# Performance work log

Measured on AMD Instinct MI355X. Metric: run time of the kernel, lower is better.

The kernel has to match this reference:

```python
import jax, jax.numpy as jnp
import numpy as np

DIM = 1024
HEADS = 16
DIM_HEAD = 64
INNER = HEADS * DIM_HEAD
B, N = 2, 2048


def setup_inputs() -> dict:
    key = jax.random.key(0)
    ks = jax.random.split(key, 5)
    x = jax.random.normal(ks[0], (B, N, DIM), dtype=jnp.float32)
    ln_gamma = jnp.ones((DIM,), dtype=jnp.float32)
    ln_beta = jnp.zeros((DIM,), dtype=jnp.float32)
    # torch Linear: weight [out, in]; store as [in, out] for x @ W
    W_qkv = jax.random.normal(ks[1], (DIM, 3 * INNER), dtype=jnp.float32) * (DIM ** -0.5)
    W_out = jax.random.normal(ks[2], (INNER, DIM), dtype=jnp.float32) * (INNER ** -0.5)
    b_out = jax.random.normal(ks[3], (DIM,), dtype=jnp.float32) * 0.01
    return {"x": x, "ln_gamma": ln_gamma, "ln_beta": ln_beta,
            "W_qkv": W_qkv, "W_out": W_out, "b_out": b_out}


def reference(x, ln_gamma, ln_beta, W_qkv, W_out, b_out):
    eps = 1e-5
    scale = DIM_HEAD ** -0.5
    # LayerNorm over last dim
    mu = jnp.mean(x, axis=-1, keepdims=True)
    var = jnp.mean((x - mu) ** 2, axis=-1, keepdims=True)
    xn = (x - mu) * jax.lax.rsqrt(var + eps) * ln_gamma + ln_beta
    # QKV projection (no bias), split
    qkv = xn @ W_qkv                               # [B, N, 3*inner]
    q, k, v = jnp.split(qkv, 3, axis=-1)           # each [B, N, inner]
    def heads(t):
        return t.reshape(B, N, HEADS, DIM_HEAD).transpose(0, 2, 1, 3)  # [B, H, N, d]
    q, k, v = heads(q), heads(k), heads(v)
    dots = jnp.einsum("bhnd,bhmd->bhnm", q, k) * scale
    a = jax.nn.softmax(dots, axis=-1)
    out = jnp.einsum("bhnm,bhmd->bhnd", a, v)      # [B, H, N, d]
    out = out.transpose(0, 2, 1, 3).reshape(B, N, INNER)
    return out @ W_out + b_out                     # dropout p=0 -> identity
```

## Files before the change

kernel.cpp:

```cpp
#include <hip/hip_runtime.h>

typedef unsigned short U16;
typedef __bf16 bf16x8 __attribute__((ext_vector_type(8)));
typedef float f32x4 __attribute__((ext_vector_type(4)));
typedef float f32x16 __attribute__((ext_vector_type(16)));

__device__ inline float b2f(U16 u) {
    union { unsigned int i; float f; } v;
    v.i = ((unsigned int)u) << 16;
    return v.f;
}
__device__ inline U16 f2b(float f) {
    union { float f; unsigned int u; } v;
    v.f = f;
    unsigned int r = (v.u + 0x7fffu + ((v.u >> 16) & 1u)) >> 16;
    return (U16)r;
}

__device__ inline unsigned cvt_pk(float lo, float hi) {
    unsigned d;
    asm("v_cvt_pk_bf16_f32 %0, %1, %2" : "=v"(d) : "v"(lo), "v"(hi));
    return d;
}
__device__ inline void plswap(unsigned &a, unsigned &b) {
    asm("v_permlane32_swap_b32 %0, %1" : "+v"(a), "+v"(b));
}

__device__ inline void gld16(const void* g, void* l) {
    __builtin_amdgcn_global_load_lds(
        (const __attribute__((address_space(1))) void*)g,
        (__attribute__((address_space(3))) void*)l, 16, 0, 0);
}

__global__ void transpose2_f2b(const float* __restrict__ inA, U16* __restrict__ outA,
                               int RA, int CA,
                               const float* __restrict__ inB, U16* __restrict__ outB,
                               int RB, int CB) {
    const float* in; U16* out; int R, C;
    if (blockIdx.z == 0) { in = inA; out = outA; R = RA; C = CA; }
    else {
        if ((int)blockIdx.x * 32 >= CB) return;
        in = inB; out = outB; R = RB; C = CB;
    }
    __shared__ float tile[32][33];
    int c0 = blockIdx.x * 32, r0 = blockIdx.y * 32;
    int tx = threadIdx.x, ty = threadIdx.y;
#pragma unroll
    for (int i = 0; i < 32; i += 8)
        tile[ty + i][tx] = in[(size_t)(r0 + ty + i) * C + c0 + tx];
    __syncthreads();
#pragma unroll
    for (int i = 0; i < 32; i += 8)
        out[(size_t)(c0 + ty + i) * R + r0 + tx] = f2b(tile[tx][ty + i]);
}

__global__ __launch_bounds__(256) void ln_kernel(const float* __restrict__ x,
                                                 const float* __restrict__ gamma,
                                                 const float* __restrict__ beta,
                                                 U16* __restrict__ xn) {
    int row = blockIdx.x;
    int t = threadIdx.x;
    float4 raw = ((const float4*)(x + (size_t)row * 1024))[t];
    float v[4] = { raw.x, raw.y, raw.z, raw.w };
    float s = v[0] + v[1] + v[2] + v[3];
    float s2 = v[0] * v[0] + v[1] * v[1] + v[2] * v[2] + v[3] * v[3];
#pragma unroll
    for (int off = 32; off >= 1; off >>= 1) {
        s  += __shfl_xor(s,  off);
        s2 += __shfl_xor(s2, off);
    }
    __shared__ float red[8];
    if ((t & 63) == 0) { red[(t >> 6) * 2] = s; red[(t >> 6) * 2 + 1] = s2; }
    __syncthreads();
    float S  = red[0] + red[2] + red[4] + red[6];
    float S2 = red[1] + red[3] + red[5] + red[7];
    float mu = S * (1.0f / 1024.0f);
    float var = S2 * (1.0f / 1024.0f) - mu * mu;
    float rstd = rsqrtf(var + 1e-5f);
    float4 g4 = ((const float4*)gamma)[t];
    float4 b4 = ((const float4*)beta)[t];
    ushort4 o;
    o.x = f2b((v[0] - mu) * rstd * g4.x + b4.x);
    o.y = f2b((v[1] - mu) * rstd * g4.y + b4.y);
    o.z = f2b((v[2] - mu) * rstd * g4.z + b4.z);
    o.w = f2b((v[3] - mu) * rstd * g4.w + b4.w);
    ((ushort4*)(xn + (size_t)row * 1024))[t] = o;
}

template <typename OutT>
__global__ __launch_bounds__(256) void gemm_bt(const U16* __restrict__ A,
                                               const U16* __restrict__ Bt,
                                               const float* __restrict__ bias,
                                               OutT* __restrict__ C,
                                               U16* __restrict__ vT,
                                               int M, int N, int K) {
    __shared__ __align__(16) U16 As[128 * 32];
    __shared__ __align__(16) U16 Bs[128 * 32];
    const int m0 = blockIdx.y * 128, n0 = blockIdx.x * 128;
    const int t = threadIdx.x;
    const int wave = t >> 6, lane = t & 63, l15 = lane & 15, quad = lane >> 4;
    const int wm = (wave >> 1) * 64, wn = (wave & 1) * 64;

    f32x4 acc[4][4];
#pragma unroll
    for (int i = 0; i < 4; i++)
#pragma unroll
        for (int j = 0; j < 4; j++)
            acc[i][j] = (f32x4){0.f, 0.f, 0.f, 0.f};

    const int c0i = t, c1i = 256 + t;
    const int r0 = c0i >> 2, kq0 = c0i & 3;
    const int r1 = c1i >> 2, kq1 = c1i & 3;

    for (int k0 = 0; k0 < K; k0 += 32) {
        gld16(&A[(size_t)(m0 + r0) * K + k0 + kq0 * 8], &As[c0i * 8]);
        gld16(&Bt[(size_t)(n0 + r0) * K + k0 + kq0 * 8], &Bs[c0i * 8]);
        gld16(&A[(size_t)(m0 + r1) * K + k0 + kq1 * 8], &As[c1i * 8]);
        gld16(&Bt[(size_t)(n0 + r1) * K + k0 + kq1 * 8], &Bs[c1i * 8]);
        __syncthreads();
        bf16x8 af[4], bfr[4];
#pragma unroll
        for (int i = 0; i < 4; i++)
            af[i] = *(const bf16x8*)&As[(wm + i * 16 + l15) * 32 + quad * 8];
#pragma unroll
        for (int j = 0; j < 4; j++)
            bfr[j] = *(const bf16x8*)&Bs[(wn + j * 16 + l15) * 32 + quad * 8];
#pragma unroll
        for (int i = 0; i < 4; i++)
#pragma unroll
            for (int j = 0; j < 4; j++)
                acc[i][j] = __builtin_amdgcn_mfma_f32_16x16x32_bf16(
                    af[i], bfr[j], acc[i][j], 0, 0, 0);
        __syncthreads();
    }
    if (vT && n0 >= 2048) {
#pragma unroll
        for (int i = 0; i < 4; i++) {
#pragma unroll
            for (int j = 0; j < 4; j++) {
                int col = n0 + wn + j * 16 + l15 - 2048;
                int hh = col >> 6, dd = col & 63;
                int row0 = m0 + wm + i * 16 + quad * 4;
                int bb = row0 >> 11, nn = row0 & 2047;
                ushort4 st;
                st.x = f2b(acc[i][j][0]); st.y = f2b(acc[i][j][1]);
                st.z = f2b(acc[i][j][2]); st.w = f2b(acc[i][j][3]);
                *(ushort4*)&vT[((((size_t)bb * 16) + hh) * 64 + dd) * 2048 + nn] = st;
            }
        }
        return;
    }
#pragma unroll
    for (int i = 0; i < 4; i++) {
#pragma unroll
        for (int j = 0; j < 4; j++) {
            int col = n0 + wn + j * 16 + l15;
            float bv = bias ? bias[col] : 0.0f;
#pragma unroll
            for (int r = 0; r < 4; r++) {
                int row = m0 + wm + i * 16 + quad * 4 + r;
                float val = acc[i][j][r] + bv;
                if constexpr (sizeof(OutT) == 4)
                    C[(size_t)row * N + col] = val;
                else
                    C[(size_t)row * N + col] = f2b(val);
            }
        }
    }
}

__global__ __launch_bounds__(256) void gemm_bt2(const U16* __restrict__ A,
                                                const U16* __restrict__ Bt,
                                                const float* __restrict__ bias,
                                                float* __restrict__ C,
                                                int M, int N, int K) {
    __shared__ __align__(16) U16 As[64 * 32];
    __shared__ __align__(16) U16 Bs[128 * 32];
    const int m0 = blockIdx.y * 64, n0 = blockIdx.x * 128;
    const int t = threadIdx.x;
    const int wave = t >> 6, lane = t & 63, l15 = lane & 15, quad = lane >> 4;
    const int wm = (wave >> 1) * 32, wn = (wave & 1) * 64;

    f32x4 acc[2][4];
#pragma unroll
    for (int i = 0; i < 2; i++)
#pragma unroll
        for (int j = 0; j < 4; j++)
            acc[i][j] = (f32x4){0.f, 0.f, 0.f, 0.f};

    const int rA = t >> 2, kqA = t & 3;

    for (int k0 = 0; k0 < K; k0 += 32) {
        gld16(&A[(size_t)(m0 + rA) * K + k0 + kqA * 8], &As[t * 8]);
        gld16(&Bt[(size_t)(n0 + rA) * K + k0 + kqA * 8], &Bs[t * 8]);
        gld16(&Bt[(size_t)(n0 + 64 + rA) * K + k0 + kqA * 8], &Bs[(256 + t) * 8]);
        __syncthreads();
        bf16x8 af[2], bfr[4];
#pragma unroll
        for (int i = 0; i < 2; i++)
            af[i] = *(const bf16x8*)&As[(wm + i * 16 + l15) * 32 + quad * 8];
#pragma unroll
        for (int j = 0; j < 4; j++)
            bfr[j] = *(const bf16x8*)&Bs[(wn + j * 16 + l15) * 32 + quad * 8];
#pragma unroll
        for (int i = 0; i < 2; i++)
#pragma unroll
            for (int j = 0; j < 4; j++)
                acc[i][j] = __builtin_amdgcn_mfma_f32_16x16x32_bf16(
                    af[i], bfr[j], acc[i][j], 0, 0, 0);
        __syncthreads();
    }
#pragma unroll
    for (int i = 0; i < 2; i++) {
#pragma unroll
        for (int j = 0; j < 4; j++) {
            int col = n0 + wn + j * 16 + l15;
            float bv = bias[col];
#pragma unroll
            for (int r = 0; r < 4; r++) {
                int row = m0 + wm + i * 16 + quad * 4 + r;
                C[(size_t)row * N + col] = acc[i][j][r] + bv;
            }
        }
    }
}

__global__ __launch_bounds__(256) void attn_kernel(const U16* __restrict__ qkv,
                                                   const U16* __restrict__ vT,
                                                   U16* __restrict__ attn_out) {
    const int p = blockIdx.x;
    const int xcd = p & 7;
    const int slot = p >> 3;
    const int bh = ((slot & 3) << 3) | xcd;
    const int qt = slot >> 2;
    const int b = bh >> 4, h = bh & 15;
    const int t = threadIdx.x;
    const int wave = t >> 6, lane = t & 63;
    const int l31 = lane & 31, hi = lane >> 5;
    const float sc2 = 0.125f * 1.44269504089f;

    __shared__ __align__(16) U16 Kt[2][64 * 64];
    __shared__ __align__(16) U16 Vt[2][64 * 64];

    const size_t base = (size_t)(b * 2048) * 3072;
    const U16* vTbh = vT + ((size_t)(b * 16 + h) * 64) * 2048;

    bf16x8 qf[4];
    {
        int qrow = qt * 128 + wave * 32 + l31;
        const U16* qp = qkv + base + (size_t)qrow * 3072 + h * 64 + hi * 8;
#pragma unroll
        for (int s = 0; s < 4; s++) {
            union { bf16x8 v; U16 u[8]; } a;
            a.v = *(const bf16x8*)&qp[s * 16];
#pragma unroll
            for (int e = 0; e < 8; e++) a.u[e] = f2b(b2f(a.u[e]) * sc2);
            qf[s] = a.v;
        }
    }

    float l4[4] = { 0.f, 0.f, 0.f, 0.f };
    f32x16 oacc[2];
#pragma unroll
    for (int db = 0; db < 2; db++)
#pragma unroll
        for (int r = 0; r < 16; r++)
            oacc[db][r] = 0.0f;

    const int c0 = t, c1 = 256 + t;
    const int row0 = c0 >> 3, oct0 = (c0 & 7) ^ (row0 & 7);
    const int row1 = c1 >> 3, oct1 = (c1 & 7) ^ (row1 & 7);

    gld16(&qkv[base + (size_t)row0 * 3072 + 1024 + h * 64 + oct0 * 8], &Kt[0][c0 * 8]);
    gld16(&qkv[base + (size_t)row1 * 3072 + 1024 + h * 64 + oct1 * 8], &Kt[0][c1 * 8]);
    gld16(&vTbh[(size_t)row0 * 2048 + oct0 * 8], &Vt[0][c0 * 8]);
    gld16(&vTbh[(size_t)row1 * 2048 + oct1 * 8], &Vt[0][c1 * 8]);
    __syncthreads();

    auto step = [&](const U16* KtC, const U16* VtC, U16* KtN, U16* VtN, int nt) {
        gld16(&qkv[base + (size_t)(nt * 64 + row0) * 3072 + 1024 + h * 64 + oct0 * 8], &KtN[c0 * 8]);
        gld16(&qkv[base + (size_t)(nt * 64 + row1) * 3072 + 1024 + h * 64 + oct1 * 8], &KtN[c1 * 8]);
        gld16(&vTbh[(size_t)row0 * 2048 + nt * 64 + oct0 * 8], &VtN[c0 * 8]);
        gld16(&vTbh[(size_t)row1 * 2048 + nt * 64 + oct1 * 8], &VtN[c1 * 8]);
#pragma unroll
        for (int kb = 0; kb < 2; kb++) {
            bf16x8 kf[4];
#pragma unroll
            for (int s = 0; s < 4; s++)
                kf[s] = *(const bf16x8*)&KtC[(kb * 32 + l31) * 64 +
                                             (((s * 2 + hi) ^ (l31 & 7)) * 8)];
            bf16x8 vfr[2][2];
#pragma unroll
            for (int db = 0; db < 2; db++)
#pragma unroll
                for (int s = 0; s < 2; s++)
                    vfr[db][s] = *(const bf16x8*)&VtC[(db * 32 + l31) * 64 +
                                                      (((kb * 4 + s * 2 + hi) ^ (l31 & 7)) * 8)];

            f32x16 st = {0.f, 0.f, 0.f, 0.f, 0.f, 0.f, 0.f, 0.f,
                         0.f, 0.f, 0.f, 0.f, 0.f, 0.f, 0.f, 0.f};
            __builtin_amdgcn_s_setprio(1);
#pragma unroll
            for (int s = 0; s < 4; s++)
                st = __builtin_amdgcn_mfma_f32_32x32x16_bf16(kf[s], qf[s], st, 0, 0, 0);
            __builtin_amdgcn_s_setprio(0);

            float pe[16];
#pragma unroll
            for (int r = 0; r < 16; r++) {
                pe[r] = __builtin_amdgcn_exp2f(st[r]);
                l4[r & 3] += pe[r];
            }

#pragma unroll
            for (int s = 0; s < 2; s++) {
                unsigned p01 = cvt_pk(pe[s * 8 + 0], pe[s * 8 + 1]);
                unsigned p23 = cvt_pk(pe[s * 8 + 2], pe[s * 8 + 3]);
                unsigned p45 = cvt_pk(pe[s * 8 + 4], pe[s * 8 + 5]);
                unsigned p67 = cvt_pk(pe[s * 8 + 6], pe[s * 8 + 7]);
                plswap(p01, p45);
                plswap(p23, p67);
                union { unsigned u[4]; bf16x8 v; } pw;
                pw.u[0] = p01; pw.u[1] = p23; pw.u[2] = p45; pw.u[3] = p67;
                __builtin_amdgcn_s_setprio(1);
#pragma unroll
                for (int db = 0; db < 2; db++)
                    oacc[db] = __builtin_amdgcn_mfma_f32_32x32x16_bf16(
                        vfr[db][s], pw.v, oacc[db], 0, 0, 0);
                __builtin_amdgcn_s_setprio(0);
            }
        }
        __syncthreads();
    };

    for (int kt2 = 0; kt2 < 16; kt2++) {
        step(&Kt[0][0], &Vt[0][0], &Kt[1][0], &Vt[1][0], 2 * kt2 + 1);
        step(&Kt[1][0], &Vt[1][0], &Kt[0][0], &Vt[0][0], (2 * kt2 + 2) & 31);
    }

    float l_acc = (l4[0] + l4[1]) + (l4[2] + l4[3]);
    float lt = l_acc + __shfl_xor(l_acc, 32);
    float inv = 1.0f / lt;
    int qrow = b * 2048 + qt * 128 + wave * 32 + l31;
#pragma unroll
    for (int db = 0; db < 2; db++) {
#pragma unroll
        for (int g = 0; g < 4; g++) {
            ushort4 stv;
            stv.x = f2b(oacc[db][g * 4 + 0] * inv);
            stv.y = f2b(oacc[db][g * 4 + 1] * inv);
            stv.z = f2b(oacc[db][g * 4 + 2] * inv);
            stv.w = f2b(oacc[db][g * 4 + 3] * inv);
            int col = h * 64 + db * 32 + g * 8 + hi * 4;
            *(ushort4*)&attn_out[(size_t)qrow * 1024 + col] = stv;
        }
    }
}

extern "C" void kernel_launch(void* const* d_in, const int* in_sizes, int n_in,
                              void* d_out, int out_size, void* d_ws, size_t ws_size,
                              hipStream_t stream) {
    (void)in_sizes; (void)n_in; (void)out_size; (void)ws_size;
    const float* x    = (const float*)d_in[0];
    const float* g    = (const float*)d_in[1];
    const float* be   = (const float*)d_in[2];
    const float* Wqkv = (const float*)d_in[3];
    const float* Wout = (const float*)d_in[4];
    const float* bout = (const float*)d_in[5];
    float* out = (float*)d_out;
    char* ws = (char*)d_ws;

    U16* xn   = (U16*)(ws);
    U16* qkv  = (U16*)(ws + (size_t)(8u  << 20));
    U16* WqT  = (U16*)(ws + (size_t)(32u << 20));
    U16* WoT  = (U16*)(ws + (size_t)(38u << 20));
    U16* vT   = (U16*)(ws + (size_t)(40u << 20));
    U16* aout = xn;

    transpose2_f2b<<<dim3(3072 / 32, 1024 / 32, 2), dim3(32, 8), 0, stream>>>(
        Wqkv, WqT, 1024, 3072, Wout, WoT, 1024, 1024);
    ln_kernel<<<4096, 256, 0, stream>>>(x, g, be, xn);
    gemm_bt<U16><<<dim3(3072 / 128, 4096 / 128), 256, 0, stream>>>(xn, WqT, nullptr, qkv, vT, 4096, 3072, 1024);
    attn_kernel<<<dim3(512), 256, 0, stream>>>(qkv, vT, aout);
    gemm_bt2<<<dim3(1024 / 128, 4096 / 64), 256, 0, stream>>>(aout, WoT, bout, out, 4096, 1024, 1024);
}
```

Measured before the change: 198.0 us.

## Fuse prep kernels and rewrite QKV GEMM with 256x256 double-buffered tiles

```diff
diff --git a/kernel.cpp b/kernel.cpp
--- a/kernel.cpp
+++ b/kernel.cpp
@@ -32,19 +32,53 @@
         (__attribute__((address_space(3))) void*)l, 16, 0, 0);
 }
 
-__global__ void transpose2_f2b(const float* __restrict__ inA, U16* __restrict__ outA,
-                               int RA, int CA,
-                               const float* __restrict__ inB, U16* __restrict__ outB,
-                               int RB, int CB) {
-    const float* in; U16* out; int R, C;
-    if (blockIdx.z == 0) { in = inA; out = outA; R = RA; C = CA; }
-    else {
-        if ((int)blockIdx.x * 32 >= CB) return;
-        in = inB; out = outB; R = RB; C = CB;
-    }
+__global__ __launch_bounds__(256) void prep_kernel(const float* __restrict__ x,
+                                                   const float* __restrict__ gamma,
+                                                   const float* __restrict__ beta,
+                                                   U16* __restrict__ xn,
+                                                   const float* __restrict__ Wqkv,
+                                                   U16* __restrict__ WqT,
+                                                   const float* __restrict__ Wout,
+                                                   U16* __restrict__ WoT) {
+    int p = blockIdx.x;
+    int t = threadIdx.x;
+    if (p < 4096) {
+        int row = p;
+        float4 raw = ((const float4*)(x + (size_t)row * 1024))[t];
+        float v[4] = { raw.x, raw.y, raw.z, raw.w };
+        float s = v[0] + v[1] + v[2] + v[3];
+        float s2 = v[0] * v[0] + v[1] * v[1] + v[2] * v[2] + v[3] * v[3];
+#pragma unroll
+        for (int off = 32; off >= 1; off >>= 1) {
+            s  += __shfl_xor(s,  off);
+            s2 += __shfl_xor(s2, off);
+        }
+        __shared__ float red[8];
+        if ((t & 63) == 0) { red[(t >> 6) * 2] = s; red[(t >> 6) * 2 + 1] = s2; }
+        __syncthreads();
+        float S  = red[0] + red[2] + red[4] + red[6];
+        float S2 = red[1] + red[3] + red[5] + red[7];
+        float mu = S * (1.0f / 1024.0f);
+        float var = S2 * (1.0f / 1024.0f) - mu * mu;
+        float rstd = rsqrtf(var + 1e-5f);
+        float4 g4 = ((const float4*)gamma)[t];
+        float4 b4 = ((const float4*)beta)[t];
+        ushort4 o;
+        o.x = f2b((v[0] - mu) * rstd * g4.x + b4.x);
+        o.y = f2b((v[1] - mu) * rstd * g4.y + b4.y);
+        o.z = f2b((v[2] - mu) * rstd * g4.z + b4.z);
+        o.w = f2b((v[3] - mu) * rstd * g4.w + b4.w);
+        ((ushort4*)(xn + (size_t)row * 1024))[t] = o;
+        return;
+    }
+    p -= 4096;
+    const float* in; U16* out; int C, tilesx;
+    if (p < 3072) { in = Wqkv; out = WqT; C = 3072; tilesx = 96; }
+    else { p -= 3072; in = Wout; out = WoT; C = 1024; tilesx = 32; }
+    const int R = 1024;
+    int c0 = (p % tilesx) * 32, r0 = (p / tilesx) * 32;
+    int tx = t & 31, ty = t >> 5;
     __shared__ float tile[32][33];
-    int c0 = blockIdx.x * 32, r0 = blockIdx.y * 32;
-    int tx = threadIdx.x, ty = threadIdx.y;
 #pragma unroll
     for (int i = 0; i < 32; i += 8)
         tile[ty + i][tx] = in[(size_t)(r0 + ty + i) * C + c0 + tx];
@@ -54,93 +88,135 @@
         out[(size_t)(c0 + ty + i) * R + r0 + tx] = f2b(tile[tx][ty + i]);
 }
 
-__global__ __launch_bounds__(256) void ln_kernel(const float* __restrict__ x,
-                                                 const float* __restrict__ gamma,
-                                                 const float* __restrict__ beta,
-                                                 U16* __restrict__ xn) {
-    int row = blockIdx.x;
-    int t = threadIdx.x;
-    float4 raw = ((const float4*)(x + (size_t)row * 1024))[t];
-    float v[4] = { raw.x, raw.y, raw.z, raw.w };
-    float s = v[0] + v[1] + v[2] + v[3];
-    float s2 = v[0] * v[0] + v[1] * v[1] + v[2] * v[2] + v[3] * v[3];
-#pragma unroll
-    for (int off = 32; off >= 1; off >>= 1) {
-        s  += __shfl_xor(s,  off);
-        s2 += __shfl_xor(s2, off);
-    }
-    __shared__ float red[8];
-    if ((t & 63) == 0) { red[(t >> 6) * 2] = s; red[(t >> 6) * 2 + 1] = s2; }
-    __syncthreads();
-    float S  = red[0] + red[2] + red[4] + red[6];
-    float S2 = red[1] + red[3] + red[5] + red[7];
-    float mu = S * (1.0f / 1024.0f);
-    float var = S2 * (1.0f / 1024.0f) - mu * mu;
-    float rstd = rsqrtf(var + 1e-5f);
-    float4 g4 = ((const float4*)gamma)[t];
-    float4 b4 = ((const float4*)beta)[t];
-    ushort4 o;
-    o.x = f2b((v[0] - mu) * rstd * g4.x + b4.x);
-    o.y = f2b((v[1] - mu) * rstd * g4.y + b4.y);
-    o.z = f2b((v[2] - mu) * rstd * g4.z + b4.z);
-    o.w = f2b((v[3] - mu) * rstd * g4.w + b4.w);
-    ((ushort4*)(xn + (size_t)row * 1024))[t] = o;
-}
-
-template <typename OutT>
-__global__ __launch_bounds__(256) void gemm_bt(const U16* __restrict__ A,
+__global__ __launch_bounds__(512) void gemm256(const U16* __restrict__ A,
                                                const U16* __restrict__ Bt,
-                                               const float* __restrict__ bias,
-                                               OutT* __restrict__ C,
+                                               U16* __restrict__ C,
                                                U16* __restrict__ vT,
                                                int M, int N, int K) {
-    __shared__ __align__(16) U16 As[128 * 32];
-    __shared__ __align__(16) U16 Bs[128 * 32];
-    const int m0 = blockIdx.y * 128, n0 = blockIdx.x * 128;
+    __shared__ __align__(16) U16 As[2][2][128 * 64];
+    __shared__ __align__(16) U16 Bs[2][2][128 * 64];
+    const int p = blockIdx.x;
+    const int xcd = p & 7, sl = p >> 3;
+    const int by = xcd * 2 + (sl >= 12 ? 1 : 0);
+    const int bx = (sl >= 12) ? (sl - 12) : sl;
+    const int m0 = by * 256, n0 = bx * 256;
     const int t = threadIdx.x;
     const int wave = t >> 6, lane = t & 63, l15 = lane & 15, quad = lane >> 4;
-    const int wm = (wave >> 1) * 64, wn = (wave & 1) * 64;
-
-    f32x4 acc[4][4];
-#pragma unroll
-    for (int i = 0; i < 4; i++)
+    const int wm = wave >> 2, wn = wave & 3;
+
+    f32x4 acc[8][4];
+#pragma unroll
+    for (int i = 0; i < 8; i++)
 #pragma unroll
         for (int j = 0; j < 4; j++)
             acc[i][j] = (f32x4){0.f, 0.f, 0.f, 0.f};
 
-    const int c0i = t, c1i = 256 + t;
-    const int r0 = c0i >> 2, kq0 = c0i & 3;
-    const int r1 = c1i >> 2, kq1 = c1i & 3;
-
-    for (int k0 = 0; k0 < K; k0 += 32) {
-        gld16(&A[(size_t)(m0 + r0) * K + k0 + kq0 * 8], &As[c0i * 8]);
-        gld16(&Bt[(size_t)(n0 + r0) * K + k0 + kq0 * 8], &Bs[c0i * 8]);
-        gld16(&A[(size_t)(m0 + r1) * K + k0 + kq1 * 8], &As[c1i * 8]);
-        gld16(&Bt[(size_t)(n0 + r1) * K + k0 + kq1 * 8], &Bs[c1i * 8]);
-        __syncthreads();
-        bf16x8 af[4], bfr[4];
+    const int c0 = t, c1 = 512 + t;
+    const int sr0 = c0 >> 3, so0 = (c0 & 7) ^ (sr0 & 7);
+    const int sr1 = c1 >> 3, so1 = (c1 & 7) ^ (sr1 & 7);
+    const U16* Ag0 = A + (size_t)(m0 + sr0) * K + so0 * 8;
+    const U16* Ag1 = A + (size_t)(m0 + sr1) * K + so1 * 8;
+    const U16* Bg0 = Bt + (size_t)(n0 + sr0) * K + so0 * 8;
+    const U16* Bg1 = Bt + (size_t)(n0 + sr1) * K + so1 * 8;
+    const size_t hstep = (size_t)128 * K;
+
+    auto stA = [&](int kt, U16* d0, U16* d1) {
+        gld16(Ag0 + kt * 64, d0 + c0 * 8);
+        gld16(Ag1 + kt * 64, d0 + c1 * 8);
+        gld16(Ag0 + hstep + kt * 64, d1 + c0 * 8);
+        gld16(Ag1 + hstep + kt * 64, d1 + c1 * 8);
+    };
+    auto stB = [&](int kt, U16* d0, U16* d1) {
+        gld16(Bg0 + kt * 64, d0 + c0 * 8);
+        gld16(Bg1 + kt * 64, d0 + c1 * 8);
+        gld16(Bg0 + hstep + kt * 64, d1 + c0 * 8);
+        gld16(Bg1 + hstep + kt * 64, d1 + c1 * 8);
+    };
+
+    const int slot0 = quad ^ (l15 & 7);
+    const int slot1 = (4 + quad) ^ (l15 & 7);
+    const int aoff0 = l15 * 64 + slot0 * 8, aoff1 = l15 * 64 + slot1 * 8;
+    const int bbase = (wn & 1) * 64 * 64;
+    const int boff0 = bbase + aoff0, boff1 = bbase + aoff1;
+    const int nk = K >> 6;
+
+    auto ktile = [&](const U16* Ac0, const U16* Ac1, const U16* Bc0, const U16* Bc1,
+                     U16* An0, U16* An1, U16* Bn0, U16* Bn1, int kt) {
+        const bool nx = (kt + 1) < nk;
+        if (nx) {
+            stA(kt + 1, An0, An1);
+            asm volatile("s_waitcnt vmcnt(4)" ::: "memory");
+        } else {
+            asm volatile("s_waitcnt vmcnt(0)" ::: "memory");
+        }
+        __builtin_amdgcn_s_barrier();
+        asm volatile("" ::: "memory");
+        const U16* Ah = wm ? Ac1 : Ac0;
+        const U16* Bh = (wn & 2) ? Bc1 : Bc0;
+        bf16x8 bfr[4][2], af[4][2];
+#pragma unroll
+        for (int j = 0; j < 4; j++) {
+            bfr[j][0] = *(const bf16x8*)&Bh[j * 16 * 64 + boff0];
+            bfr[j][1] = *(const bf16x8*)&Bh[j * 16 * 64 + boff1];
+        }
+#pragma unroll
+        for (int i = 0; i < 4; i++) {
+            af[i][0] = *(const bf16x8*)&Ah[i * 16 * 64 + aoff0];
+            af[i][1] = *(const bf16x8*)&Ah[i * 16 * 64 + aoff1];
+        }
+        if (nx) stB(kt + 1, Bn0, Bn1);
+        __builtin_amdgcn_s_setprio(1);
 #pragma unroll
         for (int i = 0; i < 4; i++)
-            af[i] = *(const bf16x8*)&As[(wm + i * 16 + l15) * 32 + quad * 8];
-#pragma unroll
-        for (int j = 0; j < 4; j++)
-            bfr[j] = *(const bf16x8*)&Bs[(wn + j * 16 + l15) * 32 + quad * 8];
+#pragma unroll
+            for (int j = 0; j < 4; j++) {
+                acc[i][j] = __builtin_amdgcn_mfma_f32_16x16x32_bf16(af[i][0], bfr[j][0], acc[i][j], 0, 0, 0);
+                acc[i][j] = __builtin_amdgcn_mfma_f32_16x16x32_bf16(af[i][1], bfr[j][1], acc[i][j], 0, 0, 0);
+            }
+        __builtin_amdgcn_s_setprio(0);
+        asm volatile("" ::: "memory");
+        __builtin_amdgcn_s_barrier();
+        asm volatile("" ::: "memory");
+#pragma unroll
+        for (int i = 0; i < 4; i++) {
+            af[i][0] = *(const bf16x8*)&Ah[(4 + i) * 16 * 64 + aoff0];
+            af[i][1] = *(const bf16x8*)&Ah[(4 + i) * 16 * 64 + aoff1];
+        }
+        __builtin_amdgcn_s_setprio(1);
 #pragma unroll
         for (int i = 0; i < 4; i++)
 #pragma unroll
-            for (int j = 0; j < 4; j++)
-                acc[i][j] = __builtin_amdgcn_mfma_f32_16x16x32_bf16(
-                    af[i], bfr[j], acc[i][j], 0, 0, 0);
-        __syncthreads();
-    }
+            for (int j = 0; j < 4; j++) {
+                acc[4 + i][j] = __builtin_amdgcn_mfma_f32_16x16x32_bf16(af[i][0], bfr[j][0], acc[4 + i][j], 0, 0, 0);
+                acc[4 + i][j] = __builtin_amdgcn_mfma_f32_16x16x32_bf16(af[i][1], bfr[j][1], acc[4 + i][j], 0, 0, 0);
+            }
+        __builtin_amdgcn_s_setprio(0);
+        asm volatile("" ::: "memory");
+        __builtin_amdgcn_s_barrier();
+        asm volatile("" ::: "memory");
+    };
+
+    stA(0, &As[0][0][0], &As[0][1][0]);
+    stB(0, &Bs[0][0][0], &Bs[0][1][0]);
+    asm volatile("s_waitcnt vmcnt(0)" ::: "memory");
+    __builtin_amdgcn_s_barrier();
+    asm volatile("" ::: "memory");
+
+    for (int kt = 0; kt < nk; kt += 2) {
+        ktile(&As[0][0][0], &As[0][1][0], &Bs[0][0][0], &Bs[0][1][0],
+              &As[1][0][0], &As[1][1][0], &Bs[1][0][0], &Bs[1][1][0], kt);
+        ktile(&As[1][0][0], &As[1][1][0], &Bs[1][0][0], &Bs[1][1][0],
+              &As[0][0][0], &As[0][1][0], &Bs[0][0][0], &Bs[0][1][0], kt + 1);
+    }
+
     if (vT && n0 >= 2048) {
 #pragma unroll
-        for (int i = 0; i < 4; i++) {
+        for (int i = 0; i < 8; i++) {
 #pragma unroll
             for (int j = 0; j < 4; j++) {
-                int col = n0 + wn + j * 16 + l15 - 2048;
+                int col = n0 + wn * 64 + j * 16 + l15 - 2048;
                 int hh = col >> 6, dd = col & 63;
-                int row0 = m0 + wm + i * 16 + quad * 4;
+                int row0 = m0 + wm * 128 + i * 16 + quad * 4;
                 int bb = row0 >> 11, nn = row0 & 2047;
                 ushort4 st;
                 st.x = f2b(acc[i][j][0]); st.y = f2b(acc[i][j][1]);
@@ -151,19 +227,14 @@
         return;
     }
 #pragma unroll
-    for (int i = 0; i < 4; i++) {
+    for (int i = 0; i < 8; i++) {
 #pragma unroll
         for (int j = 0; j < 4; j++) {
-            int col = n0 + wn + j * 16 + l15;
-            float bv = bias ? bias[col] : 0.0f;
+            int col = n0 + wn * 64 + j * 16 + l15;
 #pragma unroll
             for (int r = 0; r < 4; r++) {
-                int row = m0 + wm + i * 16 + quad * 4 + r;
-                float val = acc[i][j][r] + bv;
-                if constexpr (sizeof(OutT) == 4)
-                    C[(size_t)row * N + col] = val;
-                else
-                    C[(size_t)row * N + col] = f2b(val);
+                int row = m0 + wm * 128 + i * 16 + quad * 4 + r;
+                C[(size_t)row * N + col] = f2b(acc[i][j][r]);
             }
         }
     }
@@ -377,10 +448,8 @@
     U16* vT   = (U16*)(ws + (size_t)(40u << 20));
     U16* aout = xn;
 
-    transpose2_f2b<<<dim3(3072 / 32, 1024 / 32, 2), dim3(32, 8), 0, stream>>>(
-        Wqkv, WqT, 1024, 3072, Wout, WoT, 1024, 1024);
-    ln_kernel<<<4096, 256, 0, stream>>>(x, g, be, xn);
-    gemm_bt<U16><<<dim3(3072 / 128, 4096 / 128), 256, 0, stream>>>(xn, WqT, nullptr, qkv, vT, 4096, 3072, 1024);
-    attn_kernel<<<dim3(512), 256, 0, stream>>>(qkv, vT, aout);
+    prep_kernel<<<8192, 256, 0, stream>>>(x, g, be, xn, Wqkv, WqT, Wout, WoT);
+    gemm256<<<192, 512, 0, stream>>>(xn, WqT, qkv, vT, 4096, 3072, 1024);
+    attn_kernel<<<512, 256, 0, stream>>>(qkv, vT, aout);
     gemm_bt2<<<dim3(1024 / 128, 4096 / 64), 256, 0, stream>>>(aout, WoT, bout, out, 4096, 1024, 1024);
 }
```

New measurement: 193.4 us. 2.3% less time.
